# Kernel optimization log

Measured on AMD Instinct MI355X. Metric: run time of the kernel, lower is better.

The kernel has to match this reference:

```python
import jax, jax.numpy as jnp
import numpy as np

NUM_HEADS = 16
DIM_EMBED = 1024
DIM_K = DIM_EMBED // NUM_HEADS


def setup_inputs() -> dict:
    key = jax.random.key(0)
    ks = jax.random.split(key, 11)
    B, S, D = 2, 2048, DIM_EMBED
    scale = 1.0 / np.sqrt(D)
    inp = {
        "query": jax.random.normal(ks[0], (B, S, D), dtype=jnp.float32),
        "key": jax.random.normal(ks[1], (B, S, D), dtype=jnp.float32),
        "value": jax.random.normal(ks[2], (B, S, D), dtype=jnp.float32),
        # torch nn.Linear weights: [out_features, in_features], y = x @ W.T + b
        "Wq": jax.random.normal(ks[3], (D, D), dtype=jnp.float32) * scale,
        "bq": jnp.zeros((D,), dtype=jnp.float32),
        "Wk": jax.random.normal(ks[4], (D, D), dtype=jnp.float32) * scale,
        "bk": jnp.zeros((D,), dtype=jnp.float32),
        "Wv": jax.random.normal(ks[5], (D, D), dtype=jnp.float32) * scale,
        "bv": jnp.zeros((D,), dtype=jnp.float32),
        "Wo": jax.random.normal(ks[6], (D, D), dtype=jnp.float32) * scale,
        "bo": jnp.zeros((D,), dtype=jnp.float32),
    }
    return inp


def _split_heads(x):
    B, S, D = x.shape
    return x.reshape(B, S, NUM_HEADS, DIM_K).transpose(0, 2, 1, 3)  # [B,H,S,dk]


def reference(query, key, value, Wq, bq, Wk, bk, Wv, bv, Wo, bo):
    q = _split_heads(query @ Wq.T + bq)   # [B,H,S,dk]
    k = _split_heads(key @ Wk.T + bk)
    v = _split_heads(value @ Wv.T + bv)
    # reactivity = q @ k^T, scaled AFTER matmul as in the original
    reactivity = jnp.einsum("bhsd,bhtd->bhst", q, k)
    attention_score = jax.nn.softmax(reactivity / np.sqrt(DIM_K), axis=-1)
    blended = jnp.einsum("bhst,bhtd->bhsd", attention_score, v)  # [B,H,S,dk]
    B, H, S, dk = blended.shape
    blended = blended.transpose(0, 2, 1, 3).reshape(B, S, H * dk)
    out = blended @ Wo.T + bo
    return out, attention_score
```

## Files before the change

kernel.cpp:

```cpp
#include <hip/hip_runtime.h>
#include <stdint.h>

#define BATCH 2
#define SEQ   2048
#define DEMB  1024
#define NHEAD 16
#define DK    64
#define NTOK  (BATCH * SEQ)
#define OUT_ELEMS ((size_t)NTOK * DEMB)

typedef __bf16 bf16x8 __attribute__((ext_vector_type(8)));
typedef float  f32x4  __attribute__((ext_vector_type(4)));

union FragU { uint4 u; bf16x8 b; };

__device__ __forceinline__ unsigned short f2bf(float f) {
  union { float f; unsigned u; } v; v.f = f;
  unsigned r = v.u + 0x7fffu + ((v.u >> 16) & 1u);
  return (unsigned short)(r >> 16);
}

__global__ __launch_bounds__(256) void k_proj(
    const float* __restrict__ Xq, const float* __restrict__ Xk, const float* __restrict__ Xv,
    const float* __restrict__ Wq, const float* __restrict__ bq,
    const float* __restrict__ Wk, const float* __restrict__ bk,
    const float* __restrict__ Wv, const float* __restrict__ bv,
    unsigned short* __restrict__ qh, unsigned short* __restrict__ kh,
    unsigned short* __restrict__ vt)
{
  const int p = blockIdx.z;
  const float* __restrict__ X    = (p == 0) ? Xq : (p == 1) ? Xk : Xv;
  const float* __restrict__ W    = (p == 0) ? Wq : (p == 1) ? Wk : Wv;
  const float* __restrict__ bias = (p == 0) ? bq : (p == 1) ? bk : bv;

  __shared__ unsigned short As[128][72];
  __shared__ unsigned short Bs[128][72];

  const int tid  = threadIdx.x;
  const int lane = tid & 63;
  const int w    = tid >> 6;
  const int wm   = (w & 1) * 64;
  const int wn   = (w >> 1) * 64;
  const int l15  = lane & 15;
  const int quad = lane >> 4;

  const int row0 = blockIdx.x * 128;
  const int col0 = blockIdx.y * 128;

  f32x4 acc[4][4];
#pragma unroll
  for (int mi = 0; mi < 4; ++mi)
#pragma unroll
    for (int ni = 0; ni < 4; ++ni) acc[mi][ni] = {0.f, 0.f, 0.f, 0.f};

  for (int kk = 0; kk < DEMB; kk += 64) {
#pragma unroll
    for (int r8 = 0; r8 < 8; ++r8) {
      int row = r8 * 16 + (tid >> 4);
      int c4  = tid & 15;
      float4 a = *(const float4*)&X[(size_t)(row0 + row) * DEMB + kk + c4 * 4];
      ushort4 pa; pa.x = f2bf(a.x); pa.y = f2bf(a.y); pa.z = f2bf(a.z); pa.w = f2bf(a.w);
      *(ushort4*)&As[row][c4 * 4] = pa;
      float4 b = *(const float4*)&W[(size_t)(col0 + row) * DEMB + kk + c4 * 4];
      ushort4 pb; pb.x = f2bf(b.x); pb.y = f2bf(b.y); pb.z = f2bf(b.z); pb.w = f2bf(b.w);
      *(ushort4*)&Bs[row][c4 * 4] = pb;
    }
    __syncthreads();
#pragma unroll
    for (int k0 = 0; k0 < 64; k0 += 32) {
      FragU af[4], bfr[4];
#pragma unroll
      for (int mi = 0; mi < 4; ++mi)
        af[mi].u = *(const uint4*)&As[wm + mi * 16 + l15][k0 + quad * 8];
#pragma unroll
      for (int ni = 0; ni < 4; ++ni)
        bfr[ni].u = *(const uint4*)&Bs[wn + ni * 16 + l15][k0 + quad * 8];
#pragma unroll
      for (int mi = 0; mi < 4; ++mi)
#pragma unroll
        for (int ni = 0; ni < 4; ++ni)
          acc[mi][ni] = __builtin_amdgcn_mfma_f32_16x16x32_bf16(af[mi].b, bfr[ni].b, acc[mi][ni], 0, 0, 0);
    }
    __syncthreads();
  }

#pragma unroll
  for (int mi = 0; mi < 4; ++mi) {
#pragma unroll
    for (int ni = 0; ni < 4; ++ni) {
      int o = col0 + wn + ni * 16 + l15;
      float bv_ = bias[o];
      int h_ = o >> 6, d_ = o & 63;
#pragma unroll
      for (int i = 0; i < 4; ++i) {
        int t  = row0 + wm + mi * 16 + quad * 4 + i;
        int b_ = t >> 11, s_ = t & 2047;
        unsigned short val = f2bf(acc[mi][ni][i] + bv_);
        if (p == 0)
          qh[(((size_t)b_ * NHEAD + h_) * SEQ + s_) * DK + d_] = val;
        else if (p == 1)
          kh[(((size_t)b_ * NHEAD + h_) * SEQ + s_) * DK + d_] = val;
        else
          vt[(((size_t)b_ * NHEAD + h_) * DK + d_) * SEQ + s_] = val;
      }
    }
  }
}

__global__ __launch_bounds__(256) void k_attn(
    const unsigned short* __restrict__ qh, const unsigned short* __restrict__ kh,
    const unsigned short* __restrict__ vt, unsigned short* __restrict__ blended,
    float* __restrict__ Pout)
{
  const int bh = blockIdx.y;
  const int s0 = blockIdx.x * 64;
  const size_t hoff = (size_t)bh * SEQ * DK;

  __shared__ unsigned short Qs[64][72];
  __shared__ unsigned short Ks[64][72];
  __shared__ unsigned short Ps[64][72];
  __shared__ float rowpart[4][64];
  __shared__ float recipS[64];

  const int tid  = threadIdx.x;
  const int lane = tid & 63;
  const int w    = tid >> 6;
  const int l15  = lane & 15;
  const int quad = lane >> 4;

#pragma unroll
  for (int r = 0; r < 2; ++r) {
    int idx = tid + r * 256;
    int row = idx >> 3, c = (idx & 7) * 8;
    uint4 v = *(const uint4*)&qh[hoff + (size_t)(s0 + row) * DK + c];
    *(uint4*)&Qs[row][c] = v;
  }

  float rs[4][4];
#pragma unroll
  for (int mi = 0; mi < 4; ++mi)
#pragma unroll
    for (int i = 0; i < 4; ++i) rs[mi][i] = 0.f;

  for (int t0 = 0; t0 < SEQ; t0 += 64) {
    __syncthreads();
#pragma unroll
    for (int r = 0; r < 2; ++r) {
      int idx = tid + r * 256;
      int row = idx >> 3, c = (idx & 7) * 8;
      uint4 v = *(const uint4*)&kh[hoff + (size_t)(t0 + row) * DK + c];
      *(uint4*)&Ks[row][c] = v;
    }
    __syncthreads();
    FragU bfr[2];
#pragma unroll
    for (int k0 = 0; k0 < 2; ++k0)
      bfr[k0].u = *(const uint4*)&Ks[w * 16 + l15][k0 * 32 + quad * 8];
#pragma unroll
    for (int mi = 0; mi < 4; ++mi) {
      f32x4 a = {0.f, 0.f, 0.f, 0.f};
#pragma unroll
      for (int k0 = 0; k0 < 2; ++k0) {
        FragU af; af.u = *(const uint4*)&Qs[mi * 16 + l15][k0 * 32 + quad * 8];
        a = __builtin_amdgcn_mfma_f32_16x16x32_bf16(af.b, bfr[k0].b, a, 0, 0, 0);
      }
#pragma unroll
      for (int i = 0; i < 4; ++i) rs[mi][i] += __expf(a[i] * 0.125f);
    }
  }

#pragma unroll
  for (int mi = 0; mi < 4; ++mi)
#pragma unroll
    for (int i = 0; i < 4; ++i) {
      float v = rs[mi][i];
      v += __shfl_xor(v, 1); v += __shfl_xor(v, 2);
      v += __shfl_xor(v, 4); v += __shfl_xor(v, 8);
      rs[mi][i] = v;
    }
  if (l15 == 0) {
#pragma unroll
    for (int mi = 0; mi < 4; ++mi)
#pragma unroll
      for (int i = 0; i < 4; ++i) rowpart[w][mi * 16 + quad * 4 + i] = rs[mi][i];
  }
  __syncthreads();
  if (tid < 64)
    recipS[tid] = 1.0f / (rowpart[0][tid] + rowpart[1][tid] + rowpart[2][tid] + rowpart[3][tid]);
  __syncthreads();
  float rcp[4][4];
#pragma unroll
  for (int mi = 0; mi < 4; ++mi)
#pragma unroll
    for (int i = 0; i < 4; ++i) rcp[mi][i] = recipS[mi * 16 + quad * 4 + i];

  f32x4 accpv[4];
#pragma unroll
  for (int mi = 0; mi < 4; ++mi) accpv[mi] = {0.f, 0.f, 0.f, 0.f};

  for (int t0 = 0; t0 < SEQ; t0 += 64) {
    __syncthreads();
#pragma unroll
    for (int r = 0; r < 2; ++r) {
      int idx = tid + r * 256;
      int row = idx >> 3, c = (idx & 7) * 8;
      uint4 v = *(const uint4*)&kh[hoff + (size_t)(t0 + row) * DK + c];
      *(uint4*)&Ks[row][c] = v;
    }
    __syncthreads();
    FragU bfr[2];
#pragma unroll
    for (int k0 = 0; k0 < 2; ++k0)
      bfr[k0].u = *(const uint4*)&Ks[w * 16 + l15][k0 * 32 + quad * 8];
#pragma unroll
    for (int mi = 0; mi < 4; ++mi) {
      f32x4 a = {0.f, 0.f, 0.f, 0.f};
#pragma unroll
      for (int k0 = 0; k0 < 2; ++k0) {
        FragU af; af.u = *(const uint4*)&Qs[mi * 16 + l15][k0 * 32 + quad * 8];
        a = __builtin_amdgcn_mfma_f32_16x16x32_bf16(af.b, bfr[k0].b, a, 0, 0, 0);
      }
#pragma unroll
      for (int i = 0; i < 4; ++i) {
        float e = __expf(a[i] * 0.125f) * rcp[mi][i];
        int row = mi * 16 + quad * 4 + i;
        int col = t0 + w * 16 + l15;
        Pout[((size_t)bh * SEQ + s0 + row) * SEQ + col] = e;
        Ps[row][w * 16 + l15] = f2bf(e);
      }
    }
    __syncthreads();
    FragU bpv[2];
#pragma unroll
    for (int k0 = 0; k0 < 2; ++k0)
      bpv[k0].u = *(const uint4*)&vt[hoff + (size_t)(w * 16 + l15) * SEQ + t0 + k0 * 32 + quad * 8];
#pragma unroll
    for (int mi = 0; mi < 4; ++mi) {
#pragma unroll
      for (int k0 = 0; k0 < 2; ++k0) {
        FragU apv; apv.u = *(const uint4*)&Ps[mi * 16 + l15][k0 * 32 + quad * 8];
        accpv[mi] = __builtin_amdgcn_mfma_f32_16x16x32_bf16(apv.b, bpv[k0].b, accpv[mi], 0, 0, 0);
      }
    }
  }

  const int b_ = bh >> 4, h_ = bh & 15;
#pragma unroll
  for (int mi = 0; mi < 4; ++mi)
#pragma unroll
    for (int i = 0; i < 4; ++i) {
      int row   = mi * 16 + quad * 4 + i;
      int token = b_ * SEQ + s0 + row;
      int d     = w * 16 + l15;
      blended[(size_t)token * DEMB + h_ * DK + d] = f2bf(accpv[mi][i]);
    }
}

__global__ __launch_bounds__(256) void k_outproj(
    const unsigned short* __restrict__ blended, const float* __restrict__ Wo,
    const float* __restrict__ bo, float* __restrict__ out)
{
  __shared__ unsigned short As[128][72];
  __shared__ unsigned short Bs[128][72];

  const int tid  = threadIdx.x;
  const int lane = tid & 63;
  const int w    = tid >> 6;
  const int wm   = (w & 1) * 64;
  const int wn   = (w >> 1) * 64;
  const int l15  = lane & 15;
  const int quad = lane >> 4;

  const int row0 = blockIdx.x * 128;
  const int col0 = blockIdx.y * 128;

  f32x4 acc[4][4];
#pragma unroll
  for (int mi = 0; mi < 4; ++mi)
#pragma unroll
    for (int ni = 0; ni < 4; ++ni) acc[mi][ni] = {0.f, 0.f, 0.f, 0.f};

  for (int kk = 0; kk < DEMB; kk += 64) {
#pragma unroll
    for (int r4 = 0; r4 < 4; ++r4) {
      int row = r4 * 32 + (tid >> 3);
      int c   = (tid & 7) * 8;
      uint4 v = *(const uint4*)&blended[(size_t)(row0 + row) * DEMB + kk + c];
      *(uint4*)&As[row][c] = v;
    }
#pragma unroll
    for (int r8 = 0; r8 < 8; ++r8) {
      int row = r8 * 16 + (tid >> 4);
      int c4  = tid & 15;
      float4 b = *(const float4*)&Wo[(size_t)(col0 + row) * DEMB + kk + c4 * 4];
      ushort4 pb; pb.x = f2bf(b.x); pb.y = f2bf(b.y); pb.z = f2bf(b.z); pb.w = f2bf(b.w);
      *(ushort4*)&Bs[row][c4 * 4] = pb;
    }
    __syncthreads();
#pragma unroll
    for (int k0 = 0; k0 < 64; k0 += 32) {
      FragU af[4], bfr[4];
#pragma unroll
      for (int mi = 0; mi < 4; ++mi)
        af[mi].u = *(const uint4*)&As[wm + mi * 16 + l15][k0 + quad * 8];
#pragma unroll
      for (int ni = 0; ni < 4; ++ni)
        bfr[ni].u = *(const uint4*)&Bs[wn + ni * 16 + l15][k0 + quad * 8];
#pragma unroll
      for (int mi = 0; mi < 4; ++mi)
#pragma unroll
        for (int ni = 0; ni < 4; ++ni)
          acc[mi][ni] = __builtin_amdgcn_mfma_f32_16x16x32_bf16(af[mi].b, bfr[ni].b, acc[mi][ni], 0, 0, 0);
    }
    __syncthreads();
  }

#pragma unroll
  for (int mi = 0; mi < 4; ++mi)
#pragma unroll
    for (int ni = 0; ni < 4; ++ni) {
      int o = col0 + wn + ni * 16 + l15;
      float bv_ = bo[o];
#pragma unroll
      for (int i = 0; i < 4; ++i) {
        int t = row0 + wm + mi * 16 + quad * 4 + i;
        out[(size_t)t * DEMB + o] = acc[mi][ni][i] + bv_;
      }
    }
}

extern "C" void kernel_launch(void* const* d_in, const int* in_sizes, int n_in,
                              void* d_out, int out_size, void* d_ws, size_t ws_size,
                              hipStream_t stream) {
  const float* Xq = (const float*)d_in[0];
  const float* Xk = (const float*)d_in[1];
  const float* Xv = (const float*)d_in[2];
  const float* Wq = (const float*)d_in[3];
  const float* bq = (const float*)d_in[4];
  const float* Wk = (const float*)d_in[5];
  const float* bk = (const float*)d_in[6];
  const float* Wv = (const float*)d_in[7];
  const float* bv = (const float*)d_in[8];
  const float* Wo = (const float*)d_in[9];
  const float* bo = (const float*)d_in[10];

  float* out  = (float*)d_out;
  float* Pout = out + OUT_ELEMS;

  unsigned short* qh      = (unsigned short*)d_ws;
  unsigned short* kh      = qh + OUT_ELEMS;
  unsigned short* vt      = kh + OUT_ELEMS;
  unsigned short* blended = vt + OUT_ELEMS;

  k_proj<<<dim3(32, 8, 3), 256, 0, stream>>>(Xq, Xk, Xv, Wq, bq, Wk, bk, Wv, bv, qh, kh, vt);
  k_attn<<<dim3(SEQ / 64, BATCH * NHEAD), 256, 0, stream>>>(qh, kh, vt, blended, Pout);
  k_outproj<<<dim3(32, 8), 256, 0, stream>>>(blended, Wo, bo, out);
}
```

Baseline: 819.3 us.

## Pre-convert inputs to bf16, use direct global-to-LDS loads, vectorize stores

```diff
diff --git a/kernel.cpp b/kernel.cpp
--- a/kernel.cpp
+++ b/kernel.cpp
@@ -11,7 +11,6 @@
 
 typedef __bf16 bf16x8 __attribute__((ext_vector_type(8)));
 typedef float  f32x4  __attribute__((ext_vector_type(4)));
-
 union FragU { uint4 u; bf16x8 b; };
 
 __device__ __forceinline__ unsigned short f2bf(float f) {
@@ -20,21 +19,56 @@
   return (unsigned short)(r >> 16);
 }
 
+__device__ __forceinline__ void gll16(const void* g, void* l) {
+  __builtin_amdgcn_global_load_lds(
+      (const __attribute__((address_space(1))) void*)g,
+      (__attribute__((address_space(3))) void*)l, 16, 0, 0);
+}
+
+__global__ __launch_bounds__(256) void k_cvt(
+    const float* __restrict__ q, const float* __restrict__ k, const float* __restrict__ v,
+    const float* __restrict__ wq, const float* __restrict__ wk,
+    const float* __restrict__ wv, const float* __restrict__ wo,
+    unsigned short* __restrict__ dq, unsigned short* __restrict__ dk,
+    unsigned short* __restrict__ dv, unsigned short* __restrict__ dwq,
+    unsigned short* __restrict__ dwk, unsigned short* __restrict__ dwv,
+    unsigned short* __restrict__ dwo)
+{
+  const int t = blockIdx.y;
+  const float* s; unsigned short* d; int n4;
+  switch (t) {
+    case 0: s = q;  d = dq;  n4 = NTOK * DEMB / 4; break;
+    case 1: s = k;  d = dk;  n4 = NTOK * DEMB / 4; break;
+    case 2: s = v;  d = dv;  n4 = NTOK * DEMB / 4; break;
+    case 3: s = wq; d = dwq; n4 = DEMB * DEMB / 4; break;
+    case 4: s = wk; d = dwk; n4 = DEMB * DEMB / 4; break;
+    case 5: s = wv; d = dwv; n4 = DEMB * DEMB / 4; break;
+    default: s = wo; d = dwo; n4 = DEMB * DEMB / 4; break;
+  }
+  for (int i = blockIdx.x * 256 + threadIdx.x; i < n4; i += gridDim.x * 256) {
+    float4 f = ((const float4*)s)[i];
+    ushort4 o; o.x = f2bf(f.x); o.y = f2bf(f.y); o.z = f2bf(f.z); o.w = f2bf(f.w);
+    ((ushort4*)d)[i] = o;
+  }
+}
+
 __global__ __launch_bounds__(256) void k_proj(
-    const float* __restrict__ Xq, const float* __restrict__ Xk, const float* __restrict__ Xv,
-    const float* __restrict__ Wq, const float* __restrict__ bq,
-    const float* __restrict__ Wk, const float* __restrict__ bk,
-    const float* __restrict__ Wv, const float* __restrict__ bv,
+    const unsigned short* __restrict__ Xqb, const unsigned short* __restrict__ Xkb,
+    const unsigned short* __restrict__ Xvb,
+    const unsigned short* __restrict__ Wqb, const unsigned short* __restrict__ Wkb,
+    const unsigned short* __restrict__ Wvb,
+    const float* __restrict__ bq, const float* __restrict__ bk, const float* __restrict__ bv,
     unsigned short* __restrict__ qh, unsigned short* __restrict__ kh,
-    unsigned short* __restrict__ vt)
+    unsigned short* __restrict__ vh)
 {
   const int p = blockIdx.z;
-  const float* __restrict__ X    = (p == 0) ? Xq : (p == 1) ? Xk : Xv;
-  const float* __restrict__ W    = (p == 0) ? Wq : (p == 1) ? Wk : Wv;
-  const float* __restrict__ bias = (p == 0) ? bq : (p == 1) ? bk : bv;
-
-  __shared__ unsigned short As[128][72];
-  __shared__ unsigned short Bs[128][72];
+  const unsigned short* __restrict__ X = (p == 0) ? Xqb : (p == 1) ? Xkb : Xvb;
+  const unsigned short* __restrict__ W = (p == 0) ? Wqb : (p == 1) ? Wkb : Wvb;
+  const float* __restrict__ bias       = (p == 0) ? bq  : (p == 1) ? bk  : bv;
+  unsigned short* __restrict__ dst     = (p == 0) ? qh  : (p == 1) ? kh  : vh;
+
+  __shared__ unsigned short As[128][64];
+  __shared__ unsigned short Bs[128][64];
 
   const int tid  = threadIdx.x;
   const int lane = tid & 63;
@@ -44,8 +78,8 @@
   const int l15  = lane & 15;
   const int quad = lane >> 4;
 
-  const int row0 = blockIdx.x * 128;
-  const int col0 = blockIdx.y * 128;
+  const int o0  = blockIdx.x * 128;
+  const int t0b = blockIdx.y * 128;
 
   f32x4 acc[4][4];
 #pragma unroll
@@ -55,15 +89,11 @@
 
   for (int kk = 0; kk < DEMB; kk += 64) {
 #pragma unroll
-    for (int r8 = 0; r8 < 8; ++r8) {
-      int row = r8 * 16 + (tid >> 4);
-      int c4  = tid & 15;
-      float4 a = *(const float4*)&X[(size_t)(row0 + row) * DEMB + kk + c4 * 4];
-      ushort4 pa; pa.x = f2bf(a.x); pa.y = f2bf(a.y); pa.z = f2bf(a.z); pa.w = f2bf(a.w);
-      *(ushort4*)&As[row][c4 * 4] = pa;
-      float4 b = *(const float4*)&W[(size_t)(col0 + row) * DEMB + kk + c4 * 4];
-      ushort4 pb; pb.x = f2bf(b.x); pb.y = f2bf(b.y); pb.z = f2bf(b.z); pb.w = f2bf(b.w);
-      *(ushort4*)&Bs[row][c4 * 4] = pb;
+    for (int r = 0; r < 4; ++r) {
+      int idx = tid + r * 256;
+      int row = idx >> 3, c = (idx & 7) * 8;
+      gll16(&W[(size_t)(o0 + row) * DEMB + kk + c], (unsigned short*)As + idx * 8);
+      gll16(&X[(size_t)(t0b + row) * DEMB + kk + c], (unsigned short*)Bs + idx * 8);
     }
     __syncthreads();
 #pragma unroll
@@ -86,24 +116,44 @@
 
 #pragma unroll
   for (int mi = 0; mi < 4; ++mi) {
+    const int ob = o0 + wm + mi * 16 + quad * 4;
+    const float4 bi = *(const float4*)&bias[ob];
+    const int h_ = ob >> 6, db = ob & 63;
 #pragma unroll
     for (int ni = 0; ni < 4; ++ni) {
-      int o = col0 + wn + ni * 16 + l15;
-      float bv_ = bias[o];
-      int h_ = o >> 6, d_ = o & 63;
-#pragma unroll
-      for (int i = 0; i < 4; ++i) {
-        int t  = row0 + wm + mi * 16 + quad * 4 + i;
-        int b_ = t >> 11, s_ = t & 2047;
-        unsigned short val = f2bf(acc[mi][ni][i] + bv_);
-        if (p == 0)
-          qh[(((size_t)b_ * NHEAD + h_) * SEQ + s_) * DK + d_] = val;
-        else if (p == 1)
-          kh[(((size_t)b_ * NHEAD + h_) * SEQ + s_) * DK + d_] = val;
-        else
-          vt[(((size_t)b_ * NHEAD + h_) * DK + d_) * SEQ + s_] = val;
-      }
-    }
+      int token = t0b + wn + ni * 16 + l15;
+      int b_ = token >> 11, s_ = token & 2047;
+      ushort4 ov;
+      ov.x = f2bf(acc[mi][ni][0] + bi.x);
+      ov.y = f2bf(acc[mi][ni][1] + bi.y);
+      ov.z = f2bf(acc[mi][ni][2] + bi.z);
+      ov.w = f2bf(acc[mi][ni][3] + bi.w);
+      *(ushort4*)&dst[(((size_t)b_ * NHEAD + h_) * SEQ + s_) * DK + db] = ov;
+    }
+  }
+}
+
+__global__ __launch_bounds__(256) void k_vt(const unsigned short* __restrict__ vh,
+                                            unsigned short* __restrict__ vt)
+{
+  const int bh = blockIdx.y, s0 = blockIdx.x * 64;
+  const size_t hoff = (size_t)bh * SEQ * DK;
+  __shared__ unsigned short Ls[64][72];
+  const int tid = threadIdx.x;
+#pragma unroll
+  for (int r = 0; r < 2; ++r) {
+    int idx = tid + r * 256, row = idx >> 3, c = (idx & 7) * 8;
+    uint4 v = *(const uint4*)&vh[hoff + (size_t)(s0 + row) * DK + c];
+    *(uint4*)&Ls[row][c] = v;
+  }
+  __syncthreads();
+#pragma unroll
+  for (int r = 0; r < 2; ++r) {
+    int idx = tid + r * 256, d = idx >> 3, c = (idx & 7) * 8;
+    unsigned short tmp[8];
+#pragma unroll
+    for (int j = 0; j < 8; ++j) tmp[j] = Ls[c + j][d];
+    *(uint4*)&vt[hoff + (size_t)d * SEQ + s0 + c] = *(const uint4*)tmp;
   }
 }
 
@@ -116,8 +166,9 @@
   const int s0 = blockIdx.x * 64;
   const size_t hoff = (size_t)bh * SEQ * DK;
 
-  __shared__ unsigned short Qs[64][72];
-  __shared__ unsigned short Ks[64][72];
+  __shared__ unsigned short Qs[64][64];
+  __shared__ unsigned short Ks[64][64];
+  __shared__ unsigned short Vs[64][64];
   __shared__ unsigned short Ps[64][72];
   __shared__ float rowpart[4][64];
   __shared__ float recipS[64];
@@ -128,71 +179,52 @@
   const int l15  = lane & 15;
   const int quad = lane >> 4;
 
-#pragma unroll
-  for (int r = 0; r < 2; ++r) {
-    int idx = tid + r * 256;
-    int row = idx >> 3, c = (idx & 7) * 8;
-    uint4 v = *(const uint4*)&qh[hoff + (size_t)(s0 + row) * DK + c];
-    *(uint4*)&Qs[row][c] = v;
-  }
-
-  float rs[4][4];
+  gll16(&qh[hoff + (size_t)s0 * DK + (size_t)tid * 8], (unsigned short*)Qs + tid * 8);
+  gll16(&qh[hoff + (size_t)s0 * DK + (size_t)(tid + 256) * 8], (unsigned short*)Qs + (tid + 256) * 8);
+  __syncthreads();
+
+  FragU qf[4][2];
 #pragma unroll
   for (int mi = 0; mi < 4; ++mi)
 #pragma unroll
-    for (int i = 0; i < 4; ++i) rs[mi][i] = 0.f;
-
+    for (int k0 = 0; k0 < 2; ++k0)
+      qf[mi][k0].u = *(const uint4*)&Qs[mi * 16 + l15][k0 * 32 + quad * 8];
+
+  float rs[4] = {0.f, 0.f, 0.f, 0.f};
   for (int t0 = 0; t0 < SEQ; t0 += 64) {
     __syncthreads();
-#pragma unroll
-    for (int r = 0; r < 2; ++r) {
-      int idx = tid + r * 256;
-      int row = idx >> 3, c = (idx & 7) * 8;
-      uint4 v = *(const uint4*)&kh[hoff + (size_t)(t0 + row) * DK + c];
-      *(uint4*)&Ks[row][c] = v;
-    }
-    __syncthreads();
-    FragU bfr[2];
-#pragma unroll
-    for (int k0 = 0; k0 < 2; ++k0)
-      bfr[k0].u = *(const uint4*)&Ks[w * 16 + l15][k0 * 32 + quad * 8];
+    gll16(&kh[hoff + (size_t)t0 * DK + (size_t)tid * 8], (unsigned short*)Ks + tid * 8);
+    gll16(&kh[hoff + (size_t)t0 * DK + (size_t)(tid + 256) * 8], (unsigned short*)Ks + (tid + 256) * 8);
+    __syncthreads();
+    FragU kf[2];
+    kf[0].u = *(const uint4*)&Ks[w * 16 + l15][quad * 8];
+    kf[1].u = *(const uint4*)&Ks[w * 16 + l15][32 + quad * 8];
 #pragma unroll
     for (int mi = 0; mi < 4; ++mi) {
       f32x4 a = {0.f, 0.f, 0.f, 0.f};
-#pragma unroll
-      for (int k0 = 0; k0 < 2; ++k0) {
-        FragU af; af.u = *(const uint4*)&Qs[mi * 16 + l15][k0 * 32 + quad * 8];
-        a = __builtin_amdgcn_mfma_f32_16x16x32_bf16(af.b, bfr[k0].b, a, 0, 0, 0);
-      }
-#pragma unroll
-      for (int i = 0; i < 4; ++i) rs[mi][i] += __expf(a[i] * 0.125f);
-    }
-  }
-
-#pragma unroll
-  for (int mi = 0; mi < 4; ++mi)
-#pragma unroll
-    for (int i = 0; i < 4; ++i) {
-      float v = rs[mi][i];
-      v += __shfl_xor(v, 1); v += __shfl_xor(v, 2);
-      v += __shfl_xor(v, 4); v += __shfl_xor(v, 8);
-      rs[mi][i] = v;
-    }
-  if (l15 == 0) {
-#pragma unroll
-    for (int mi = 0; mi < 4; ++mi)
-#pragma unroll
-      for (int i = 0; i < 4; ++i) rowpart[w][mi * 16 + quad * 4 + i] = rs[mi][i];
+      a = __builtin_amdgcn_mfma_f32_16x16x32_bf16(kf[0].b, qf[mi][0].b, a, 0, 0, 0);
+      a = __builtin_amdgcn_mfma_f32_16x16x32_bf16(kf[1].b, qf[mi][1].b, a, 0, 0, 0);
+#pragma unroll
+      for (int i = 0; i < 4; ++i) rs[mi] += __expf(a[i] * 0.125f);
+    }
+  }
+#pragma unroll
+  for (int mi = 0; mi < 4; ++mi) {
+    float v = rs[mi];
+    v += __shfl_xor(v, 16); v += __shfl_xor(v, 32);
+    rs[mi] = v;
+  }
+  if (lane < 16) {
+#pragma unroll
+    for (int mi = 0; mi < 4; ++mi) rowpart[w][mi * 16 + lane] = rs[mi];
   }
   __syncthreads();
   if (tid < 64)
     recipS[tid] = 1.0f / (rowpart[0][tid] + rowpart[1][tid] + rowpart[2][tid] + rowpart[3][tid]);
   __syncthreads();
-  float rcp[4][4];
-#pragma unroll
-  for (int mi = 0; mi < 4; ++mi)
-#pragma unroll
-    for (int i = 0; i < 4; ++i) rcp[mi][i] = recipS[mi * 16 + quad * 4 + i];
+  float rcp[4];
+#pragma unroll
+  for (int mi = 0; mi < 4; ++mi) rcp[mi] = recipS[mi * 16 + l15];
 
   f32x4 accpv[4];
 #pragma unroll
@@ -200,68 +232,59 @@
 
   for (int t0 = 0; t0 < SEQ; t0 += 64) {
     __syncthreads();
-#pragma unroll
-    for (int r = 0; r < 2; ++r) {
-      int idx = tid + r * 256;
-      int row = idx >> 3, c = (idx & 7) * 8;
-      uint4 v = *(const uint4*)&kh[hoff + (size_t)(t0 + row) * DK + c];
-      *(uint4*)&Ks[row][c] = v;
-    }
-    __syncthreads();
-    FragU bfr[2];
-#pragma unroll
-    for (int k0 = 0; k0 < 2; ++k0)
-      bfr[k0].u = *(const uint4*)&Ks[w * 16 + l15][k0 * 32 + quad * 8];
+    gll16(&kh[hoff + (size_t)t0 * DK + (size_t)tid * 8], (unsigned short*)Ks + tid * 8);
+    gll16(&kh[hoff + (size_t)t0 * DK + (size_t)(tid + 256) * 8], (unsigned short*)Ks + (tid + 256) * 8);
+    gll16(&vt[hoff + (size_t)(tid >> 3) * SEQ + t0 + (tid & 7) * 8], (unsigned short*)Vs + tid * 8);
+    gll16(&vt[hoff + (size_t)((tid + 256) >> 3) * SEQ + t0 + (tid & 7) * 8], (unsigned short*)Vs + (tid + 256) * 8);
+    __syncthreads();
+    FragU kf[2];
+    kf[0].u = *(const uint4*)&Ks[w * 16 + l15][quad * 8];
+    kf[1].u = *(const uint4*)&Ks[w * 16 + l15][32 + quad * 8];
 #pragma unroll
     for (int mi = 0; mi < 4; ++mi) {
       f32x4 a = {0.f, 0.f, 0.f, 0.f};
-#pragma unroll
-      for (int k0 = 0; k0 < 2; ++k0) {
-        FragU af; af.u = *(const uint4*)&Qs[mi * 16 + l15][k0 * 32 + quad * 8];
-        a = __builtin_amdgcn_mfma_f32_16x16x32_bf16(af.b, bfr[k0].b, a, 0, 0, 0);
-      }
-#pragma unroll
-      for (int i = 0; i < 4; ++i) {
-        float e = __expf(a[i] * 0.125f) * rcp[mi][i];
-        int row = mi * 16 + quad * 4 + i;
-        int col = t0 + w * 16 + l15;
-        Pout[((size_t)bh * SEQ + s0 + row) * SEQ + col] = e;
-        Ps[row][w * 16 + l15] = f2bf(e);
-      }
-    }
-    __syncthreads();
-    FragU bpv[2];
-#pragma unroll
-    for (int k0 = 0; k0 < 2; ++k0)
-      bpv[k0].u = *(const uint4*)&vt[hoff + (size_t)(w * 16 + l15) * SEQ + t0 + k0 * 32 + quad * 8];
+      a = __builtin_amdgcn_mfma_f32_16x16x32_bf16(kf[0].b, qf[mi][0].b, a, 0, 0, 0);
+      a = __builtin_amdgcn_mfma_f32_16x16x32_bf16(kf[1].b, qf[mi][1].b, a, 0, 0, 0);
+      float e0 = __expf(a[0] * 0.125f) * rcp[mi];
+      float e1 = __expf(a[1] * 0.125f) * rcp[mi];
+      float e2 = __expf(a[2] * 0.125f) * rcp[mi];
+      float e3 = __expf(a[3] * 0.125f) * rcp[mi];
+      float4 p4; p4.x = e0; p4.y = e1; p4.z = e2; p4.w = e3;
+      *(float4*)&Pout[((size_t)bh * SEQ + s0 + mi * 16 + l15) * SEQ + t0 + w * 16 + quad * 4] = p4;
+      ushort4 pb; pb.x = f2bf(e0); pb.y = f2bf(e1); pb.z = f2bf(e2); pb.w = f2bf(e3);
+      *(ushort4*)&Ps[mi * 16 + l15][w * 16 + quad * 4] = pb;
+    }
+    __syncthreads();
+    FragU vf[2];
+    vf[0].u = *(const uint4*)&Vs[w * 16 + l15][quad * 8];
+    vf[1].u = *(const uint4*)&Vs[w * 16 + l15][32 + quad * 8];
 #pragma unroll
     for (int mi = 0; mi < 4; ++mi) {
-#pragma unroll
-      for (int k0 = 0; k0 < 2; ++k0) {
-        FragU apv; apv.u = *(const uint4*)&Ps[mi * 16 + l15][k0 * 32 + quad * 8];
-        accpv[mi] = __builtin_amdgcn_mfma_f32_16x16x32_bf16(apv.b, bpv[k0].b, accpv[mi], 0, 0, 0);
-      }
+      FragU pf0, pf1;
+      pf0.u = *(const uint4*)&Ps[mi * 16 + l15][quad * 8];
+      pf1.u = *(const uint4*)&Ps[mi * 16 + l15][32 + quad * 8];
+      accpv[mi] = __builtin_amdgcn_mfma_f32_16x16x32_bf16(vf[0].b, pf0.b, accpv[mi], 0, 0, 0);
+      accpv[mi] = __builtin_amdgcn_mfma_f32_16x16x32_bf16(vf[1].b, pf1.b, accpv[mi], 0, 0, 0);
     }
   }
 
   const int b_ = bh >> 4, h_ = bh & 15;
 #pragma unroll
-  for (int mi = 0; mi < 4; ++mi)
-#pragma unroll
-    for (int i = 0; i < 4; ++i) {
-      int row   = mi * 16 + quad * 4 + i;
-      int token = b_ * SEQ + s0 + row;
-      int d     = w * 16 + l15;
-      blended[(size_t)token * DEMB + h_ * DK + d] = f2bf(accpv[mi][i]);
-    }
+  for (int mi = 0; mi < 4; ++mi) {
+    ushort4 ob;
+    ob.x = f2bf(accpv[mi][0]); ob.y = f2bf(accpv[mi][1]);
+    ob.z = f2bf(accpv[mi][2]); ob.w = f2bf(accpv[mi][3]);
+    int token = b_ * SEQ + s0 + mi * 16 + l15;
+    *(ushort4*)&blended[(size_t)token * DEMB + h_ * DK + w * 16 + quad * 4] = ob;
+  }
 }
 
 __global__ __launch_bounds__(256) void k_outproj(
-    const unsigned short* __restrict__ blended, const float* __restrict__ Wo,
+    const unsigned short* __restrict__ Wob, const unsigned short* __restrict__ blended,
     const float* __restrict__ bo, float* __restrict__ out)
 {
-  __shared__ unsigned short As[128][72];
-  __shared__ unsigned short Bs[128][72];
+  __shared__ unsigned short As[128][64];
+  __shared__ unsigned short Bs[128][64];
 
   const int tid  = threadIdx.x;
   const int lane = tid & 63;
@@ -271,8 +294,8 @@
   const int l15  = lane & 15;
   const int quad = lane >> 4;
 
-  const int row0 = blockIdx.x * 128;
-  const int col0 = blockIdx.y * 128;
+  const int o0  = blockIdx.x * 128;
+  const int t0b = blockIdx.y * 128;
 
   f32x4 acc[4][4];
 #pragma unroll
@@ -282,19 +305,11 @@
 
   for (int kk = 0; kk < DEMB; kk += 64) {
 #pragma unroll
-    for (int r4 = 0; r4 < 4; ++r4) {
-      int row = r4 * 32 + (tid >> 3);
-      int c   = (tid & 7) * 8;
-      uint4 v = *(const uint4*)&blended[(size_t)(row0 + row) * DEMB + kk + c];
-      *(uint4*)&As[row][c] = v;
-    }
-#pragma unroll
-    for (int r8 = 0; r8 < 8; ++r8) {
-      int row = r8 * 16 + (tid >> 4);
-      int c4  = tid & 15;
-      float4 b = *(const float4*)&Wo[(size_t)(col0 + row) * DEMB + kk + c4 * 4];
-      ushort4 pb; pb.x = f2bf(b.x); pb.y = f2bf(b.y); pb.z = f2bf(b.z); pb.w = f2bf(b.w);
-      *(ushort4*)&Bs[row][c4 * 4] = pb;
+    for (int r = 0; r < 4; ++r) {
+      int idx = tid + r * 256;
+      int row = idx >> 3, c = (idx & 7) * 8;
+      gll16(&Wob[(size_t)(o0 + row) * DEMB + kk + c], (unsigned short*)As + idx * 8);
+      gll16(&blended[(size_t)(t0b + row) * DEMB + kk + c], (unsigned short*)Bs + idx * 8);
     }
     __syncthreads();
 #pragma unroll
@@ -316,17 +331,20 @@
   }
 
 #pragma unroll
-  for (int mi = 0; mi < 4; ++mi)
+  for (int mi = 0; mi < 4; ++mi) {
+    const int ob = o0 + wm + mi * 16 + quad * 4;
+    const float4 bi = *(const float4*)&bo[ob];
 #pragma unroll
     for (int ni = 0; ni < 4; ++ni) {
-      int o = col0 + wn + ni * 16 + l15;
-      float bv_ = bo[o];
-#pragma unroll
-      for (int i = 0; i < 4; ++i) {
-        int t = row0 + wm + mi * 16 + quad * 4 + i;
-        out[(size_t)t * DEMB + o] = acc[mi][ni][i] + bv_;
-      }
-    }
+      int token = t0b + wn + ni * 16 + l15;
+      float4 ov;
+      ov.x = acc[mi][ni][0] + bi.x;
+      ov.y = acc[mi][ni][1] + bi.y;
+      ov.z = acc[mi][ni][2] + bi.z;
+      ov.w = acc[mi][ni][3] + bi.w;
+      *(float4*)&out[(size_t)token * DEMB + ob] = ov;
+    }
+  }
 }
 
 extern "C" void kernel_launch(void* const* d_in, const int* in_sizes, int n_in,
@@ -347,12 +365,24 @@
   float* out  = (float*)d_out;
   float* Pout = out + OUT_ELEMS;
 
-  unsigned short* qh      = (unsigned short*)d_ws;
+  unsigned short* Xqb = (unsigned short*)d_ws;
+  unsigned short* Xkb = Xqb + OUT_ELEMS;
+  unsigned short* Xvb = Xkb + OUT_ELEMS;
+  unsigned short* Wqb = Xvb + OUT_ELEMS;
+  unsigned short* Wkb = Wqb + (size_t)DEMB * DEMB;
+  unsigned short* Wvb = Wkb + (size_t)DEMB * DEMB;
+  unsigned short* Wob = Wvb + (size_t)DEMB * DEMB;
+  unsigned short* qh      = Wob + (size_t)DEMB * DEMB;
   unsigned short* kh      = qh + OUT_ELEMS;
-  unsigned short* vt      = kh + OUT_ELEMS;
+  unsigned short* vh      = kh + OUT_ELEMS;
+  unsigned short* vt      = vh + OUT_ELEMS;
   unsigned short* blended = vt + OUT_ELEMS;
 
-  k_proj<<<dim3(32, 8, 3), 256, 0, stream>>>(Xq, Xk, Xv, Wq, bq, Wk, bk, Wv, bv, qh, kh, vt);
+  k_cvt<<<dim3(1024, 7), 256, 0, stream>>>(Xq, Xk, Xv, Wq, Wk, Wv, Wo,
+                                           Xqb, Xkb, Xvb, Wqb, Wkb, Wvb, Wob);
+  k_proj<<<dim3(8, 32, 3), 256, 0, stream>>>(Xqb, Xkb, Xvb, Wqb, Wkb, Wvb,
+                                             bq, bk, bv, qh, kh, vh);
+  k_vt<<<dim3(32, 32), 256, 0, stream>>>(vh, vt);
   k_attn<<<dim3(SEQ / 64, BATCH * NHEAD), 256, 0, stream>>>(qh, kh, vt, blended, Pout);
-  k_outproj<<<dim3(32, 8), 256, 0, stream>>>(blended, Wo, bo, out);
-}
+  k_outproj<<<dim3(8, 32), 256, 0, stream>>>(Wob, blended, bo, out);
+}
```

Measured after the change: 787.8 us. 3.9% less time.
